# Kernel tuning notes

Measured on AMD Instinct MI355X. Metric: run time of the kernel, lower is better.

Reference implementation:

```python
import jax, jax.numpy as jnp
import numpy as np

B, S, E, H, V = 128, 400, 512, 512, 50000


def setup_inputs() -> dict:
    key = jax.random.key(0)
    ks = jax.random.split(key, 16)
    s = 0.05  # param scale
    return {
        "embedded": jax.random.normal(ks[0], (B, E), jnp.float32),
        "hidden": jax.random.normal(ks[1], (1, B, H), jnp.float32),
        "encoder_states": jax.random.normal(ks[2], (S, B, H), jnp.float32),
        "encoder_word_idx": jax.random.randint(ks[3], (S, B), 0, V),
        "ext_vocab_size": V,
        "W_ih": jax.random.normal(ks[4], (3 * H, E), jnp.float32) * s,
        "W_hh": jax.random.normal(ks[5], (3 * H, H), jnp.float32) * s,
        "b_ih": jax.random.normal(ks[6], (3 * H,), jnp.float32) * s,
        "b_hh": jax.random.normal(ks[7], (3 * H,), jnp.float32) * s,
        "W_bil": jax.random.normal(ks[8], (1, H, H), jnp.float32) * s,
        "b_bil": jax.random.normal(ks[9], (1,), jnp.float32) * s,
        "W_out": jax.random.normal(ks[10], (V, 2 * H), jnp.float32) * s,
        "b_out": jax.random.normal(ks[11], (V,), jnp.float32) * s,
        "W_ptr": jax.random.normal(ks[12], (1, 2 * H), jnp.float32) * s,
        "b_ptr": jax.random.normal(ks[13], (1,), jnp.float32) * s,
    }


def reference(embedded, hidden, encoder_states, encoder_word_idx, ext_vocab_size,
              W_ih, W_hh, b_ih, b_hh, W_bil, b_bil, W_out, b_out, W_ptr, b_ptr):
    h = hidden[0]  # [B, H]
    # --- single-step GRU (PyTorch gate order r, z, n) ---
    gi = embedded @ W_ih.T + b_ih          # [B, 3H]
    gh = h @ W_hh.T + b_hh                 # [B, 3H]
    i_r, i_z, i_n = jnp.split(gi, 3, axis=1)
    h_r, h_z, h_n = jnp.split(gh, 3, axis=1)
    r = jax.nn.sigmoid(i_r + h_r)
    z = jax.nn.sigmoid(i_z + h_z)
    n = jnp.tanh(i_n + r * h_n)
    h_new = (1.0 - z) * n + z * h          # [B, H]
    # --- bilinear attention energy over src dim ---
    # hidden is broadcast along S, so precompute h_new @ W once.
    v = h_new @ W_bil[0]                                   # [B, H]
    energy = jnp.einsum('bh,sbh->sb', v, encoder_states) + b_bil[0]  # [S, B]
    attn = jax.nn.softmax(energy, axis=0)                  # softmax over src len
    context = jnp.einsum('sbh,sb->bh', encoder_states, attn)  # [B, H]
    combined = jnp.concatenate([h_new, context], axis=1)   # [B, 2H]
    # --- output assembly: generator softmax + pointer mix ---
    logits = combined @ W_out.T + b_out                    # [B, V]
    prob_ptr = jax.nn.sigmoid(combined @ W_ptr.T + b_ptr)  # [B, 1]
    gen = jax.nn.softmax(logits, axis=1)
    Bsz = embedded.shape[0]
    out = jnp.zeros((Bsz, ext_vocab_size), logits.dtype)
    out = out.at[:, :logits.shape[1]].set((1.0 - prob_ptr) * gen)
    idx = encoder_word_idx.T                               # [B, S]
    out = out.at[jnp.arange(Bsz)[:, None], idx].add(prob_ptr * attn.T)
    out = jnp.log(out)                                     # log_prob=True
    enc_attn = attn.T[:, :, None]                          # [B, S, 1]
    return out, h_new[None], enc_attn, prob_ptr
```

## Files before the change

### kernel.cpp

```cpp
#include <hip/hip_runtime.h>
#include <cstdint>
#include <cstddef>

typedef float f4 __attribute__((ext_vector_type(4)));
typedef float f2 __attribute__((ext_vector_type(2)));
typedef short short8 __attribute__((ext_vector_type(8)));

#define NB 128
#define NH 512
#define NS 400
#define NV 50000

__device__ __forceinline__ unsigned short f2bf(float f) {
  unsigned u = __float_as_uint(f);
  u = u + 0x7fffu + ((u >> 16) & 1u);
  return (unsigned short)(u >> 16);
}

__device__ __forceinline__ int fragidx(int m, int k) {
  int c = k >> 7;
  int t = (k >> 5) & 3;
  int q = (k >> 3) & 3;
  int o = k & 7;
  return ((((c * 4 + t) * 8 + (m >> 4)) * 64) + q * 16 + (m & 15)) * 8 + o;
}

__global__ __launch_bounds__(256) void k1_gigh(
    const float* __restrict__ emb, const float* __restrict__ hid,
    const float* __restrict__ Wih, const float* __restrict__ Whh,
    float* __restrict__ C)
{
  __shared__ float As[32 * 68];
  __shared__ float Bs[32 * 36];
  const int tid = threadIdx.x;
  const int n0g = blockIdx.x * 32;
  const int m0  = blockIdx.y * 64;
  const float* A; const float* Bm; int n0;
  if (n0g < 1536) { A = emb; Bm = Wih; n0 = n0g; }
  else            { A = hid; Bm = Whh; n0 = n0g - 1536; }
  const int mt = tid & 15, nt = tid >> 4;
  const int arow = tid >> 2, ac = tid & 3;
  const int brow = tid >> 3, bc = tid & 7;
  float acc[4][2] = {};
  for (int k0 = 0; k0 < 512; k0 += 32) {
    f4 x0 = *(const f4*)(A + (m0 + arow) * 512 + k0 + ac * 8);
    f4 x1 = *(const f4*)(A + (m0 + arow) * 512 + k0 + ac * 8 + 4);
    f4 y  = *(const f4*)(Bm + (n0 + brow) * 512 + k0 + bc * 4);
    __syncthreads();
#pragma unroll
    for (int kk = 0; kk < 4; kk++) {
      As[(ac * 8 + kk) * 68 + arow]     = x0[kk];
      As[(ac * 8 + 4 + kk) * 68 + arow] = x1[kk];
      Bs[(bc * 4 + kk) * 36 + brow]     = y[kk];
    }
    __syncthreads();
#pragma unroll
    for (int kk = 0; kk < 32; kk++) {
      f4 a = *(const f4*)(As + kk * 68 + mt * 4);
      f2 b = *(const f2*)(Bs + kk * 36 + nt * 2);
#pragma unroll
      for (int i = 0; i < 4; i++) {
        acc[i][0] += a[i] * b[0];
        acc[i][1] += a[i] * b[1];
      }
    }
  }
#pragma unroll
  for (int i = 0; i < 4; i++) {
    f2 o; o[0] = acc[i][0]; o[1] = acc[i][1];
    *(f2*)(C + (size_t)(m0 + mt * 4 + i) * 3072 + n0g + nt * 2) = o;
  }
}

__global__ __launch_bounds__(256) void k2_gates(
    const float* __restrict__ gigh, const float* __restrict__ hid,
    const float* __restrict__ bih, const float* __restrict__ bhh,
    float* __restrict__ out_h, float* __restrict__ comb,
    unsigned short* __restrict__ cbf)
{
  int i = blockIdx.x * 256 + threadIdx.x;
  int b = i >> 9, j = i & 511;
  const float* gg = gigh + b * 3072;
  float ir  = gg[j]        + bih[j];
  float iz  = gg[j + 512]  + bih[j + 512];
  float in_ = gg[j + 1024] + bih[j + 1024];
  float hr  = gg[j + 1536] + bhh[j];
  float hz  = gg[j + 2048] + bhh[j + 512];
  float hn  = gg[j + 2560] + bhh[j + 1024];
  float r = 1.f / (1.f + expf(-(ir + hr)));
  float z = 1.f / (1.f + expf(-(iz + hz)));
  float n = tanhf(in_ + r * hn);
  float hnew = (1.f - z) * n + z * hid[i];
  out_h[i] = hnew;
  comb[b * 1024 + j] = hnew;
  cbf[fragidx(b, j)] = f2bf(hnew);
}

__global__ __launch_bounds__(256) void k3_v(
    const float* __restrict__ comb, const float* __restrict__ Wbil,
    float* __restrict__ v)
{
  int i = blockIdx.x * 256 + threadIdx.x;
  int b = i >> 9, j = i & 511;
  const float* x = comb + b * 1024;
  float acc = 0.f;
#pragma unroll 8
  for (int h = 0; h < 512; h++) acc += x[h] * Wbil[h * 512 + j];
  v[i] = acc;
}

__global__ __launch_bounds__(256) void k4_energy(
    const float* __restrict__ enc, const float* __restrict__ v,
    const float* __restrict__ bbil, float* __restrict__ energy)
{
  int tid = threadIdx.x;
  int gw = blockIdx.x * 4 + (tid >> 6);
  int lane = tid & 63;
  int s = gw >> 7, b = gw & 127;
  const float* er = enc + ((size_t)(s * 128 + b)) * 512 + lane * 8;
  const float* vr = v + b * 512 + lane * 8;
  f4 e0 = *(const f4*)er, e1 = *(const f4*)(er + 4);
  f4 v0 = *(const f4*)vr, v1 = *(const f4*)(vr + 4);
  float d = e0[0]*v0[0] + e0[1]*v0[1] + e0[2]*v0[2] + e0[3]*v0[3]
          + e1[0]*v1[0] + e1[1]*v1[1] + e1[2]*v1[2] + e1[3]*v1[3];
#pragma unroll
  for (int o = 32; o; o >>= 1) d += __shfl_xor(d, o);
  if (lane == 0) energy[b * 400 + s] = d + bbil[0];
}

__global__ __launch_bounds__(256) void k4_softmax(
    float* __restrict__ energy, float* __restrict__ out_attn)
{
  __shared__ float sm[4];
  int b = blockIdx.x, tid = threadIdx.x;
  float* e = energy + b * 400;
  float e0 = (tid < 400)       ? e[tid]       : -3.4e38f;
  float e1 = (tid + 256 < 400) ? e[tid + 256] : -3.4e38f;
  float m = fmaxf(e0, e1);
#pragma unroll
  for (int o = 32; o; o >>= 1) m = fmaxf(m, __shfl_xor(m, o));
  if ((tid & 63) == 0) sm[tid >> 6] = m;
  __syncthreads();
  m = fmaxf(fmaxf(sm[0], sm[1]), fmaxf(sm[2], sm[3]));
  __syncthreads();
  float x0 = (tid < 400)       ? expf(e0 - m) : 0.f;
  float x1 = (tid + 256 < 400) ? expf(e1 - m) : 0.f;
  float s = x0 + x1;
#pragma unroll
  for (int o = 32; o; o >>= 1) s += __shfl_xor(s, o);
  if ((tid & 63) == 0) sm[tid >> 6] = s;
  __syncthreads();
  s = sm[0] + sm[1] + sm[2] + sm[3];
  float inv = 1.f / s;
  if (tid < 400)       { float a = x0 * inv; e[tid] = a;       out_attn[b * 400 + tid] = a; }
  if (tid + 256 < 400) { float a = x1 * inv; e[tid + 256] = a; out_attn[b * 400 + tid + 256] = a; }
}

__global__ __launch_bounds__(256) void k4_context(
    const float* __restrict__ enc, const float* __restrict__ attn,
    float* __restrict__ comb, unsigned short* __restrict__ cbf)
{
  __shared__ float at[400];
  int b = blockIdx.y, ht = blockIdx.x, tid = threadIdx.x;
  for (int i = tid; i < 400; i += 256) at[i] = attn[b * 400 + i];
  __syncthreads();
  int h = ht * 256 + tid;
  const float* ep = enc + (size_t)b * 512 + h;
  float acc = 0.f;
#pragma unroll 4
  for (int s = 0; s < 400; s++) acc += at[s] * ep[(size_t)s * 65536];
  comb[b * 1024 + 512 + h] = acc;
  cbf[fragidx(b, 512 + h)] = f2bf(acc);
}

__global__ __launch_bounds__(64) void k_pptr(
    const float* __restrict__ comb, const float* __restrict__ Wptr,
    const float* __restrict__ bptr, float* __restrict__ out_p,
    float* __restrict__ p)
{
  int b = blockIdx.x, lane = threadIdx.x;
  const float* x = comb + b * 1024;
  float d = 0.f;
#pragma unroll
  for (int i = 0; i < 16; i++) d += x[i * 64 + lane] * Wptr[i * 64 + lane];
#pragma unroll
  for (int o = 32; o; o >>= 1) d += __shfl_xor(d, o);
  if (lane == 0) {
    float pv = 1.f / (1.f + expf(-(d + bptr[0])));
    out_p[b] = pv;
    p[b] = pv;
  }
}

__global__ __launch_bounds__(128) void k5_logits(
    const unsigned short* __restrict__ Abf, const float* __restrict__ W,
    const float* __restrict__ bout, float* __restrict__ out)
{
  __shared__ __align__(16) unsigned short As[16384];
  const int tid = threadIdx.x;
  const int wid = tid >> 6, lane = tid & 63;
  const int quad = lane >> 4, l16 = lane & 15;
  const int vb = blockIdx.x * 64 + wid * 32;
  const int v0 = vb + l16;
  const int v1 = vb + 16 + l16;
  const size_t r0 = (size_t)(v0 < NV ? v0 : NV - 1) * 1024 + quad * 8;
  const size_t r1 = (size_t)(v1 < NV ? v1 : NV - 1) * 1024 + quad * 8;
  f4 acc0[8] = {}, acc1[8] = {};
  f4 wa0 = *(const f4*)(W + r0);
  f4 wa1 = *(const f4*)(W + r0 + 4);
  f4 wb0 = *(const f4*)(W + r1);
  f4 wb1 = *(const f4*)(W + r1 + 4);
  for (int c = 0; c < 8; c++) {
    const f4* src = (const f4*)(Abf + c * 16384);
    f4* dst = (f4*)As;
    __syncthreads();
#pragma unroll 4
    for (int j = 0; j < 16; j++) dst[j * 128 + tid] = src[j * 128 + tid];
    __syncthreads();
#pragma unroll
    for (int t = 0; t < 4; t++) {
      short8 b0, b1;
      b0[0] = (short)f2bf(wa0[0]); b0[1] = (short)f2bf(wa0[1]);
      b0[2] = (short)f2bf(wa0[2]); b0[3] = (short)f2bf(wa0[3]);
      b0[4] = (short)f2bf(wa1[0]); b0[5] = (short)f2bf(wa1[1]);
      b0[6] = (short)f2bf(wa1[2]); b0[7] = (short)f2bf(wa1[3]);
      b1[0] = (short)f2bf(wb0[0]); b1[1] = (short)f2bf(wb0[1]);
      b1[2] = (short)f2bf(wb0[2]); b1[3] = (short)f2bf(wb0[3]);
      b1[4] = (short)f2bf(wb1[0]); b1[5] = (short)f2bf(wb1[1]);
      b1[6] = (short)f2bf(wb1[2]); b1[7] = (short)f2bf(wb1[3]);
      int kn = c * 128 + (t + 1) * 32;
      if (kn < 1024) {
        wa0 = *(const f4*)(W + r0 + kn); wa1 = *(const f4*)(W + r0 + kn + 4);
        wb0 = *(const f4*)(W + r1 + kn); wb1 = *(const f4*)(W + r1 + kn + 4);
      }
      const short8* afp = (const short8*)(As + t * 4096);
#pragma unroll
      for (int mt = 0; mt < 8; mt++) {
        short8 af = afp[mt * 64 + lane];
        acc0[mt] = __builtin_amdgcn_mfma_f32_16x16x32_bf16(af, b0, acc0[mt], 0, 0, 0);
        acc1[mt] = __builtin_amdgcn_mfma_f32_16x16x32_bf16(af, b1, acc1[mt], 0, 0, 0);
      }
    }
  }
  if (v0 < NV) {
    float bias = bout[v0];
#pragma unroll
    for (int mt = 0; mt < 8; mt++)
#pragma unroll
      for (int r = 0; r < 4; r++)
        out[(size_t)(mt * 16 + quad * 4 + r) * NV + v0] = acc0[mt][r] + bias;
  }
  if (v1 < NV) {
    float bias = bout[v1];
#pragma unroll
    for (int mt = 0; mt < 8; mt++)
#pragma unroll
      for (int r = 0; r < 4; r++)
        out[(size_t)(mt * 16 + quad * 4 + r) * NV + v1] = acc1[mt][r] + bias;
  }
}

__global__ __launch_bounds__(1024) void k5_stats(
    const float* __restrict__ out, const float* __restrict__ p,
    float* __restrict__ t)
{
  __shared__ float sm[16];
  int b = blockIdx.x, tid = threadIdx.x;
  const float* L = out + (size_t)b * NV;
  float m = -3.4e38f;
  for (int vv = tid; vv < NV; vv += 1024) m = fmaxf(m, L[vv]);
#pragma unroll
  for (int o = 32; o; o >>= 1) m = fmaxf(m, __shfl_xor(m, o));
  if ((tid & 63) == 0) sm[tid >> 6] = m;
  __syncthreads();
  float M = sm[0];
#pragma unroll
  for (int i = 1; i < 16; i++) M = fmaxf(M, sm[i]);
  __syncthreads();
  float s = 0.f;
  for (int vv = tid; vv < NV; vv += 1024) s += expf(L[vv] - M);
#pragma unroll
  for (int o = 32; o; o >>= 1) s += __shfl_xor(s, o);
  if ((tid & 63) == 0) sm[tid >> 6] = s;
  __syncthreads();
  if (tid == 0) {
    float S = 0.f;
#pragma unroll
    for (int i = 0; i < 16; i++) S += sm[i];
    t[b] = -M - logf(S) + logf(1.f - p[b]);
  }
}

__global__ __launch_bounds__(256) void k5_shift(
    float* __restrict__ out, const float* __restrict__ t)
{
  int vv = blockIdx.x * 256 + threadIdx.x;
  int b = blockIdx.y;
  if (vv < NV) out[(size_t)b * NV + vv] += t[b];
}

__global__ __launch_bounds__(256) void k5_scatter(
    const int* __restrict__ idx, const float* __restrict__ p,
    const float* __restrict__ attn, float* __restrict__ out)
{
  int i = blockIdx.x * 256 + threadIdx.x;
  if (i >= NS * NB) return;
  int s = i >> 7, b = i & 127;
  float add = p[b] * attn[b * 400 + s];
  int* ai = (int*)(out + (size_t)b * NV + idx[i]);
  int cur = *ai;
  while (true) {
    float oldf = __int_as_float(cur);
    float nv = logf(expf(oldf) + add);
    int got = atomicCAS(ai, cur, __float_as_int(nv));
    if (got == cur) break;
    cur = got;
  }
}

extern "C" void kernel_launch(void* const* d_in, const int* in_sizes, int n_in,
                              void* d_out, int out_size, void* d_ws, size_t ws_size,
                              hipStream_t stream) {
  (void)in_sizes; (void)n_in; (void)out_size; (void)ws_size;
  const float* emb  = (const float*)d_in[0];
  const float* hid  = (const float*)d_in[1];
  const float* enc  = (const float*)d_in[2];
  const int*   widx = (const int*)d_in[3];
  const float* Wih  = (const float*)d_in[5];
  const float* Whh  = (const float*)d_in[6];
  const float* bih  = (const float*)d_in[7];
  const float* bhh  = (const float*)d_in[8];
  const float* Wbil = (const float*)d_in[9];
  const float* bbil = (const float*)d_in[10];
  const float* Wout = (const float*)d_in[11];
  const float* bout = (const float*)d_in[12];
  const float* Wptr = (const float*)d_in[13];
  const float* bptr = (const float*)d_in[14];

  float* out      = (float*)d_out;
  float* out_logp = out;
  float* out_h    = out + 6400000;
  float* out_attn = out + 6465536;
  float* out_p    = out + 6516736;

  float* ws   = (float*)d_ws;
  float* gigh = ws;
  float* comb = ws + 393216;
  float* vws  = ws + 524288;
  float* attn = ws + 589824;
  float* pws  = ws + 641024;
  float* tws  = ws + 641152;
  unsigned short* cbf = (unsigned short*)(ws + 641280);

  k1_gigh   <<<dim3(96, 2),   256, 0, stream>>>(emb, hid, Wih, Whh, gigh);
  k2_gates  <<<256,           256, 0, stream>>>(gigh, hid, bih, bhh, out_h, comb, cbf);
  k3_v      <<<256,           256, 0, stream>>>(comb, Wbil, vws);
  k4_energy <<<12800,         256, 0, stream>>>(enc, vws, bbil, attn);
  k4_softmax<<<128,           256, 0, stream>>>(attn, out_attn);
  k4_context<<<dim3(2, 128),  256, 0, stream>>>(enc, attn, comb, cbf);
  k_pptr    <<<128,            64, 0, stream>>>(comb, Wptr, bptr, out_p, pws);
  k5_logits <<<782,           128, 0, stream>>>(cbf, Wout, bout, out_logp);
  k5_stats  <<<128,          1024, 0, stream>>>(out_logp, pws, tws);
  k5_shift  <<<dim3(196, 128),256, 0, stream>>>(out_logp, tws);
  k5_scatter<<<200,           256, 0, stream>>>(widx, pws, attn, out_logp);
}
```

Baseline: 554.1 us.

## Fuse softmax partial stats into logits GEMM, split context reduction, batch energy rows

New measurement: 508.5 us. 1.09x faster.

```diff
diff --git a/kernel.cpp b/kernel.cpp
--- a/kernel.cpp
+++ b/kernel.cpp
@@ -10,6 +10,7 @@
 #define NH 512
 #define NS 400
 #define NV 50000
+#define NEGBIG (-3.402823466e38f)
 
 __device__ __forceinline__ unsigned short f2bf(float f) {
   unsigned u = __float_as_uint(f);
@@ -104,28 +105,42 @@
   int b = i >> 9, j = i & 511;
   const float* x = comb + b * 1024;
   float acc = 0.f;
-#pragma unroll 8
+#pragma unroll 16
   for (int h = 0; h < 512; h++) acc += x[h] * Wbil[h * 512 + j];
   v[i] = acc;
 }
 
-__global__ __launch_bounds__(256) void k4_energy(
+__global__ __launch_bounds__(128) void k4_energy(
     const float* __restrict__ enc, const float* __restrict__ v,
     const float* __restrict__ bbil, float* __restrict__ energy)
 {
   int tid = threadIdx.x;
-  int gw = blockIdx.x * 4 + (tid >> 6);
-  int lane = tid & 63;
-  int s = gw >> 7, b = gw & 127;
-  const float* er = enc + ((size_t)(s * 128 + b)) * 512 + lane * 8;
+  int wid = tid >> 6, lane = tid & 63;
+  int b = blockIdx.y;
+  int sc = blockIdx.x * 2 + wid;
   const float* vr = v + b * 512 + lane * 8;
-  f4 e0 = *(const f4*)er, e1 = *(const f4*)(er + 4);
   f4 v0 = *(const f4*)vr, v1 = *(const f4*)(vr + 4);
-  float d = e0[0]*v0[0] + e0[1]*v0[1] + e0[2]*v0[2] + e0[3]*v0[3]
-          + e1[0]*v1[0] + e1[1]*v1[1] + e1[2]*v1[2] + e1[3]*v1[3];
-#pragma unroll
-  for (int o = 32; o; o >>= 1) d += __shfl_xor(d, o);
-  if (lane == 0) energy[b * 400 + s] = d + bbil[0];
+  float e[8];
+#pragma unroll
+  for (int i = 0; i < 8; i++) {
+    int s = sc * 8 + i;
+    const float* er = enc + ((size_t)(s * 128 + b)) * 512 + lane * 8;
+    f4 e0 = *(const f4*)er, e1 = *(const f4*)(er + 4);
+    e[i] = e0[0]*v0[0] + e0[1]*v0[1] + e0[2]*v0[2] + e0[3]*v0[3]
+         + e1[0]*v1[0] + e1[1]*v1[1] + e1[2]*v1[2] + e1[3]*v1[3];
+  }
+#pragma unroll
+  for (int i = 0; i < 8; i++)
+#pragma unroll
+    for (int o = 32; o; o >>= 1) e[i] += __shfl_xor(e[i], o);
+  if (lane == 0) {
+    float bb = bbil[0];
+    f4 o0, o1;
+    o0[0] = e[0] + bb; o0[1] = e[1] + bb; o0[2] = e[2] + bb; o0[3] = e[3] + bb;
+    o1[0] = e[4] + bb; o1[1] = e[5] + bb; o1[2] = e[6] + bb; o1[3] = e[7] + bb;
+    *(f4*)(energy + b * 400 + sc * 8)     = o0;
+    *(f4*)(energy + b * 400 + sc * 8 + 4) = o1;
+  }
 }
 
 __global__ __launch_bounds__(256) void k4_softmax(
@@ -134,8 +149,8 @@
   __shared__ float sm[4];
   int b = blockIdx.x, tid = threadIdx.x;
   float* e = energy + b * 400;
-  float e0 = (tid < 400)       ? e[tid]       : -3.4e38f;
-  float e1 = (tid + 256 < 400) ? e[tid + 256] : -3.4e38f;
+  float e0 = (tid < 400)       ? e[tid]       : NEGBIG;
+  float e1 = (tid + 256 < 400) ? e[tid + 256] : NEGBIG;
   float m = fmaxf(e0, e1);
 #pragma unroll
   for (int o = 32; o; o >>= 1) m = fmaxf(m, __shfl_xor(m, o));
@@ -158,19 +173,33 @@
 
 __global__ __launch_bounds__(256) void k4_context(
     const float* __restrict__ enc, const float* __restrict__ attn,
-    float* __restrict__ comb, unsigned short* __restrict__ cbf)
-{
-  __shared__ float at[400];
-  int b = blockIdx.y, ht = blockIdx.x, tid = threadIdx.x;
-  for (int i = tid; i < 400; i += 256) at[i] = attn[b * 400 + i];
+    float* __restrict__ P)
+{
+  __shared__ float at[100];
+  int b = blockIdx.y, ht = blockIdx.x & 1, sq = blockIdx.x >> 1;
+  int tid = threadIdx.x;
+  if (tid < 100) at[tid] = attn[b * 400 + sq * 100 + tid];
   __syncthreads();
   int h = ht * 256 + tid;
-  const float* ep = enc + (size_t)b * 512 + h;
+  const float* ep = enc + (size_t)(sq * 100 * 128 + b) * 512 + h;
   float acc = 0.f;
-#pragma unroll 4
-  for (int s = 0; s < 400; s++) acc += at[s] * ep[(size_t)s * 65536];
-  comb[b * 1024 + 512 + h] = acc;
-  cbf[fragidx(b, 512 + h)] = f2bf(acc);
+#pragma unroll 10
+  for (int s = 0; s < 100; s++) acc += at[s] * ep[(size_t)s * 65536];
+  P[(size_t)((sq * 128 + b) * 2 + ht) * 256 + tid] = acc;
+}
+
+__global__ __launch_bounds__(256) void k4_ctxsum(
+    const float* __restrict__ P, float* __restrict__ comb,
+    unsigned short* __restrict__ cbf)
+{
+  int i = blockIdx.x * 256 + threadIdx.x;
+  int b = i >> 9, j = i & 511;
+  int ht = j >> 8, tt = j & 255;
+  float s = 0.f;
+#pragma unroll
+  for (int q = 0; q < 4; q++) s += P[(size_t)((q * 128 + b) * 2 + ht) * 256 + tt];
+  comb[b * 1024 + 512 + j] = s;
+  cbf[fragidx(b, 512 + j)] = f2bf(s);
 }
 
 __global__ __launch_bounds__(64) void k_pptr(
@@ -192,9 +221,10 @@
   }
 }
 
-__global__ __launch_bounds__(128) void k5_logits(
+__global__ __launch_bounds__(128, 2) void k5_logits(
     const unsigned short* __restrict__ Abf, const float* __restrict__ W,
-    const float* __restrict__ bout, float* __restrict__ out)
+    const float* __restrict__ bout, float* __restrict__ out,
+    float* __restrict__ pMS)
 {
   __shared__ __align__(16) unsigned short As[16384];
   const int tid = threadIdx.x;
@@ -203,91 +233,115 @@
   const int vb = blockIdx.x * 64 + wid * 32;
   const int v0 = vb + l16;
   const int v1 = vb + 16 + l16;
-  const size_t r0 = (size_t)(v0 < NV ? v0 : NV - 1) * 1024 + quad * 8;
-  const size_t r1 = (size_t)(v1 < NV ? v1 : NV - 1) * 1024 + quad * 8;
+  const bool ok0 = v0 < NV, ok1 = v1 < NV;
+  const size_t r0 = (size_t)(ok0 ? v0 : NV - 1) * 1024 + quad * 8;
+  const size_t r1 = (size_t)(ok1 ? v1 : NV - 1) * 1024 + quad * 8;
   f4 acc0[8] = {}, acc1[8] = {};
-  f4 wa0 = *(const f4*)(W + r0);
-  f4 wa1 = *(const f4*)(W + r0 + 4);
-  f4 wb0 = *(const f4*)(W + r1);
-  f4 wb1 = *(const f4*)(W + r1 + 4);
+  f4 w0[8], w1[8];
+#pragma unroll
+  for (int t = 0; t < 4; t++) {
+    w0[2*t]   = *(const f4*)(W + r0 + t * 32);
+    w0[2*t+1] = *(const f4*)(W + r0 + t * 32 + 4);
+    w1[2*t]   = *(const f4*)(W + r1 + t * 32);
+    w1[2*t+1] = *(const f4*)(W + r1 + t * 32 + 4);
+  }
   for (int c = 0; c < 8; c++) {
     const f4* src = (const f4*)(Abf + c * 16384);
     f4* dst = (f4*)As;
+    f4 st[16];
+#pragma unroll
+    for (int j = 0; j < 16; j++) st[j] = src[j * 128 + tid];
     __syncthreads();
-#pragma unroll 4
-    for (int j = 0; j < 16; j++) dst[j * 128 + tid] = src[j * 128 + tid];
+#pragma unroll
+    for (int j = 0; j < 16; j++) dst[j * 128 + tid] = st[j];
+    short8 B0[4], B1[4];
+#pragma unroll
+    for (int t = 0; t < 4; t++) {
+      f4 a = w0[2*t], b = w0[2*t+1], cfl = w1[2*t], d = w1[2*t+1];
+      B0[t][0] = (short)f2bf(a[0]); B0[t][1] = (short)f2bf(a[1]);
+      B0[t][2] = (short)f2bf(a[2]); B0[t][3] = (short)f2bf(a[3]);
+      B0[t][4] = (short)f2bf(b[0]); B0[t][5] = (short)f2bf(b[1]);
+      B0[t][6] = (short)f2bf(b[2]); B0[t][7] = (short)f2bf(b[3]);
+      B1[t][0] = (short)f2bf(cfl[0]); B1[t][1] = (short)f2bf(cfl[1]);
+      B1[t][2] = (short)f2bf(cfl[2]); B1[t][3] = (short)f2bf(cfl[3]);
+      B1[t][4] = (short)f2bf(d[0]); B1[t][5] = (short)f2bf(d[1]);
+      B1[t][6] = (short)f2bf(d[2]); B1[t][7] = (short)f2bf(d[3]);
+    }
+    if (c < 7) {
+      const float* p0 = W + r0 + (c + 1) * 128;
+      const float* p1 = W + r1 + (c + 1) * 128;
+#pragma unroll
+      for (int t = 0; t < 4; t++) {
+        w0[2*t]   = *(const f4*)(p0 + t * 32);
+        w0[2*t+1] = *(const f4*)(p0 + t * 32 + 4);
+        w1[2*t]   = *(const f4*)(p1 + t * 32);
+        w1[2*t+1] = *(const f4*)(p1 + t * 32 + 4);
+      }
+    }
     __syncthreads();
 #pragma unroll
     for (int t = 0; t < 4; t++) {
-      short8 b0, b1;
-      b0[0] = (short)f2bf(wa0[0]); b0[1] = (short)f2bf(wa0[1]);
-      b0[2] = (short)f2bf(wa0[2]); b0[3] = (short)f2bf(wa0[3]);
-      b0[4] = (short)f2bf(wa1[0]); b0[5] = (short)f2bf(wa1[1]);
-      b0[6] = (short)f2bf(wa1[2]); b0[7] = (short)f2bf(wa1[3]);
-      b1[0] = (short)f2bf(wb0[0]); b1[1] = (short)f2bf(wb0[1]);
-      b1[2] = (short)f2bf(wb0[2]); b1[3] = (short)f2bf(wb0[3]);
-      b1[4] = (short)f2bf(wb1[0]); b1[5] = (short)f2bf(wb1[1]);
-      b1[6] = (short)f2bf(wb1[2]); b1[7] = (short)f2bf(wb1[3]);
-      int kn = c * 128 + (t + 1) * 32;
-      if (kn < 1024) {
-        wa0 = *(const f4*)(W + r0 + kn); wa1 = *(const f4*)(W + r0 + kn + 4);
-        wb0 = *(const f4*)(W + r1 + kn); wb1 = *(const f4*)(W + r1 + kn + 4);
-      }
       const short8* afp = (const short8*)(As + t * 4096);
 #pragma unroll
       for (int mt = 0; mt < 8; mt++) {
         short8 af = afp[mt * 64 + lane];
-        acc0[mt] = __builtin_amdgcn_mfma_f32_16x16x32_bf16(af, b0, acc0[mt], 0, 0, 0);
-        acc1[mt] = __builtin_amdgcn_mfma_f32_16x16x32_bf16(af, b1, acc1[mt], 0, 0, 0);
+        acc0[mt] = __builtin_amdgcn_mfma_f32_16x16x32_bf16(af, B0[t], acc0[mt], 0, 0, 0);
+        acc1[mt] = __builtin_amdgcn_mfma_f32_16x16x32_bf16(af, B1[t], acc1[mt], 0, 0, 0);
       }
     }
   }
-  if (v0 < NV) {
-    float bias = bout[v0];
-#pragma unroll
-    for (int mt = 0; mt < 8; mt++)
-#pragma unroll
-      for (int r = 0; r < 4; r++)
-        out[(size_t)(mt * 16 + quad * 4 + r) * NV + v0] = acc0[mt][r] + bias;
-  }
-  if (v1 < NV) {
-    float bias = bout[v1];
-#pragma unroll
-    for (int mt = 0; mt < 8; mt++)
-#pragma unroll
-      for (int r = 0; r < 4; r++)
-        out[(size_t)(mt * 16 + quad * 4 + r) * NV + v1] = acc1[mt][r] + bias;
-  }
-}
-
-__global__ __launch_bounds__(1024) void k5_stats(
-    const float* __restrict__ out, const float* __restrict__ p,
+  float bias0 = ok0 ? bout[v0] : 0.f;
+  float bias1 = ok1 ? bout[v1] : 0.f;
+#pragma unroll
+  for (int mt = 0; mt < 8; mt++) {
+#pragma unroll
+    for (int r = 0; r < 4; r++) {
+      int brow = mt * 16 + quad * 4 + r;
+      float a0 = ok0 ? acc0[mt][r] + bias0 : NEGBIG;
+      float a1 = ok1 ? acc1[mt][r] + bias1 : NEGBIG;
+      if (ok0) out[(size_t)brow * NV + v0] = a0;
+      if (ok1) out[(size_t)brow * NV + v1] = a1;
+      float m = fmaxf(a0, a1);
+#pragma unroll
+      for (int o = 8; o; o >>= 1) m = fmaxf(m, __shfl_xor(m, o));
+      float s = (ok0 ? expf(a0 - m) : 0.f) + (ok1 ? expf(a1 - m) : 0.f);
+#pragma unroll
+      for (int o = 8; o; o >>= 1) s += __shfl_xor(s, o);
+      if (l16 == 0) {
+        f2 ms; ms[0] = m; ms[1] = s;
+        *(f2*)(pMS + (size_t)brow * 3200 + (blockIdx.x * 2 + wid) * 2) = ms;
+      }
+    }
+  }
+}
+
+__global__ __launch_bounds__(256) void k5_reduce(
+    const float* __restrict__ pMS, const float* __restrict__ p,
     float* __restrict__ t)
 {
-  __shared__ float sm[16];
+  __shared__ float sm[4];
   int b = blockIdx.x, tid = threadIdx.x;
-  const float* L = out + (size_t)b * NV;
-  float m = -3.4e38f;
-  for (int vv = tid; vv < NV; vv += 1024) m = fmaxf(m, L[vv]);
-#pragma unroll
-  for (int o = 32; o; o >>= 1) m = fmaxf(m, __shfl_xor(m, o));
-  if ((tid & 63) == 0) sm[tid >> 6] = m;
-  __syncthreads();
-  float M = sm[0];
-#pragma unroll
-  for (int i = 1; i < 16; i++) M = fmaxf(M, sm[i]);
-  __syncthreads();
-  float s = 0.f;
-  for (int vv = tid; vv < NV; vv += 1024) s += expf(L[vv] - M);
-#pragma unroll
-  for (int o = 32; o; o >>= 1) s += __shfl_xor(s, o);
-  if ((tid & 63) == 0) sm[tid >> 6] = s;
+  const f2* q = (const f2*)(pMS + (size_t)b * 3200);
+  float M = NEGBIG;
+  for (int i = tid; i < 1564; i += 256) M = fmaxf(M, q[i][0]);
+#pragma unroll
+  for (int o = 32; o; o >>= 1) M = fmaxf(M, __shfl_xor(M, o));
+  if ((tid & 63) == 0) sm[tid >> 6] = M;
+  __syncthreads();
+  M = fmaxf(fmaxf(sm[0], sm[1]), fmaxf(sm[2], sm[3]));
+  __syncthreads();
+  float S = 0.f;
+  for (int i = tid; i < 1564; i += 256) {
+    f2 v = q[i];
+    S += v[1] * expf(v[0] - M);
+  }
+#pragma unroll
+  for (int o = 32; o; o >>= 1) S += __shfl_xor(S, o);
+  if ((tid & 63) == 0) sm[tid >> 6] = S;
   __syncthreads();
   if (tid == 0) {
-    float S = 0.f;
-#pragma unroll
-    for (int i = 0; i < 16; i++) S += sm[i];
-    t[b] = -M - logf(S) + logf(1.f - p[b]);
+    float Sf = sm[0] + sm[1] + sm[2] + sm[3];
+    t[b] = -M - logf(Sf) + logf(1.f - p[b]);
   }
 }
 
@@ -351,16 +405,19 @@
   float* pws  = ws + 641024;
   float* tws  = ws + 641152;
   unsigned short* cbf = (unsigned short*)(ws + 641280);
-
-  k1_gigh   <<<dim3(96, 2),   256, 0, stream>>>(emb, hid, Wih, Whh, gigh);
-  k2_gates  <<<256,           256, 0, stream>>>(gigh, hid, bih, bhh, out_h, comb, cbf);
-  k3_v      <<<256,           256, 0, stream>>>(comb, Wbil, vws);
-  k4_energy <<<12800,         256, 0, stream>>>(enc, vws, bbil, attn);
-  k4_softmax<<<128,           256, 0, stream>>>(attn, out_attn);
-  k4_context<<<dim3(2, 128),  256, 0, stream>>>(enc, attn, comb, cbf);
-  k_pptr    <<<128,            64, 0, stream>>>(comb, Wptr, bptr, out_p, pws);
-  k5_logits <<<782,           128, 0, stream>>>(cbf, Wout, bout, out_logp);
-  k5_stats  <<<128,          1024, 0, stream>>>(out_logp, pws, tws);
-  k5_shift  <<<dim3(196, 128),256, 0, stream>>>(out_logp, tws);
-  k5_scatter<<<200,           256, 0, stream>>>(widx, pws, attn, out_logp);
-}
+  float* Pctx = ws + 706816;
+  float* pMS  = ws + 968960;
+
+  k1_gigh   <<<dim3(96, 2),    256, 0, stream>>>(emb, hid, Wih, Whh, gigh);
+  k2_gates  <<<256,            256, 0, stream>>>(gigh, hid, bih, bhh, out_h, comb, cbf);
+  k3_v      <<<256,            256, 0, stream>>>(comb, Wbil, vws);
+  k4_energy <<<dim3(25, 128),  128, 0, stream>>>(enc, vws, bbil, attn);
+  k4_softmax<<<128,            256, 0, stream>>>(attn, out_attn);
+  k4_context<<<dim3(8, 128),   256, 0, stream>>>(enc, attn, Pctx);
+  k4_ctxsum <<<256,            256, 0, stream>>>(Pctx, comb, cbf);
+  k_pptr    <<<128,             64, 0, stream>>>(comb, Wptr, bptr, out_p, pws);
+  k5_logits <<<782,            128, 0, stream>>>(cbf, Wout, bout, out_logp, pMS);
+  k5_reduce <<<128,            256, 0, stream>>>(pMS, pws, tws);
+  k5_shift  <<<dim3(196, 128), 256, 0, stream>>>(out_logp, tws);
+  k5_scatter<<<200,            256, 0, stream>>>(widx, pws, attn, out_logp);
+}
```
